# Optimization experiments

Hardware: AMD Instinct MI355X
Metric: run time of the kernel (lower is better)

Reference implementation:

```python
import jax, jax.numpy as jnp
import numpy as np

B, N, D = 1024, 32, 512  # graphs, node types (=nodes per graph), node_dim
EPS = 1e-5

def setup_inputs() -> dict:
    key = jax.random.key(0)
    ks = jax.random.split(key, 6)
    z = jax.random.normal(ks[0], (B, N, D), jnp.float32)
    # each graph contains every node type exactly once, in random order
    idx = jax.vmap(lambda k: jax.random.permutation(k, N))(jax.random.split(ks[1], B)).astype(jnp.int32)
    A = jax.random.normal(ks[2], (N, N), jnp.float32) / np.sqrt(N)
    W1 = jax.random.normal(ks[3], (N, D, 2 * D), jnp.float32) / np.sqrt(D)
    b1 = jnp.zeros((N, 2 * D), jnp.float32)
    W2 = jax.random.normal(ks[4], (N, 2 * D, D), jnp.float32) / np.sqrt(2 * D)
    b2 = jnp.zeros((N, D), jnp.float32)
    gamma = jnp.ones((D,), jnp.float32)
    beta = jnp.zeros((D,), jnp.float32)
    return dict(z=z, idx=idx, A=A, W1=W1, b1=b1, W2=W2, b2=b2, gamma=gamma, beta=beta)

def _layernorm(x, g, b):
    m = jnp.mean(x, axis=-1, keepdims=True)
    v = jnp.var(x, axis=-1, keepdims=True)
    return (x - m) * jax.lax.rsqrt(v + EPS) * g + b

def reference(z, idx, A, W1, b1, W2, b2, gamma, beta):
    # per-graph submatrix of global A: A_sub[b] = A[node_index, node_index]
    A_sub = A[idx[:, :, None], idx[:, None, :]]            # [B,K,K]
    # Az[b] = A_sub[b].T @ z[b]
    Az = jnp.einsum('bkj,bkd->bjd', A_sub, z)              # [B,K,D]
    Az = _layernorm(Az, gamma, beta)
    # route node of type t to expert t: inv[b,t] = position of type t in graph b
    inv = jnp.argsort(idx, axis=1)                         # [B,N]
    x = jnp.take_along_axis(Az, inv[:, :, None], axis=1)   # [B,N,D] type-ordered
    # per-type 2-layer MLP experts (Linear -> ELU -> Linear), dropout in eval mode
    h = jax.nn.elu(jnp.einsum('bnd,ndh->bnh', x, W1) + b1) # [B,N,2D]
    y = jnp.einsum('bnh,nhd->bnd', h, W2) + b2             # [B,N,D]
    # scatter back to node order: node j in graph b has type idx[b,j]
    mix = jnp.take_along_axis(y, idx[:, :, None].astype(jnp.int32), axis=1)
    return mix + Az
```

## Files before the change

### kernel.cpp

```cpp
#include <hip/hip_runtime.h>
#include <hip/hip_bf16.h>
#include <math.h>

#define B_  1024
#define N_  32
#define D_  512
#define EPS_ 1e-5f

typedef __attribute__((ext_vector_type(8))) short bf16x8;
typedef __attribute__((ext_vector_type(4))) float f32x4;
using bf16 = __hip_bfloat16;
typedef unsigned int u32;
typedef const u32 __attribute__((address_space(1)))* gp_t;
typedef u32 __attribute__((address_space(3)))* sp_t;

static __device__ __forceinline__ void gload16(const void* g, void* s) {
  __builtin_amdgcn_global_load_lds((gp_t)g, (sp_t)s, 16, 0, 0);
}
static __device__ __forceinline__ void bar() {
  asm volatile("s_barrier" ::: "memory");
}

static __device__ __forceinline__ unsigned short f2bf(float f) {
  union { float f; u32 u; } c; c.f = f;
  u32 r = c.u + 0x7fff + ((c.u >> 16) & 1);
  return (unsigned short)(r >> 16);
}
static __device__ __forceinline__ float bf2f(unsigned short h) {
  union { u32 u; float f; } c; c.u = ((u32)h) << 16;
  return c.f;
}

__global__ __launch_bounds__(256) void transpose_cast_kernel(
    const float* __restrict__ in, bf16* __restrict__ out, int R, int C) {
  __shared__ unsigned short tile[64][65];
  const size_t mat = (size_t)blockIdx.z * (size_t)R * (size_t)C;
  const float* inp = in + mat;
  bf16* outp = out + mat;
  const int c0 = blockIdx.x * 64, r0 = blockIdx.y * 64;
  const int tr = threadIdx.x >> 4;
  const int tc = (threadIdx.x & 15) * 4;
#pragma unroll
  for (int i = 0; i < 4; ++i) {
    const int r = tr + i * 16;
    float4 v = *(const float4*)&inp[(size_t)(r0 + r) * C + c0 + tc];
    tile[r][tc + 0] = f2bf(v.x);
    tile[r][tc + 1] = f2bf(v.y);
    tile[r][tc + 2] = f2bf(v.z);
    tile[r][tc + 3] = f2bf(v.w);
  }
  __syncthreads();
#pragma unroll
  for (int i = 0; i < 2; ++i) {
    const int chunk = i * 256 + threadIdx.x;
    const int c = chunk >> 3, r8 = (chunk & 7) * 8;
    union { bf16x8 v; unsigned short u[8]; } pk;
#pragma unroll
    for (int k = 0; k < 8; ++k) pk.u[k] = tile[r8 + k][c];
    *(bf16x8*)&outp[(size_t)(c0 + c) * R + r0 + r8] = pk.v;
  }
}

__global__ __launch_bounds__(256) void mix_ln_kernel(
    const float* __restrict__ z, const int* __restrict__ idx,
    const float* __restrict__ A, const float* __restrict__ gamma,
    const float* __restrict__ beta, bf16* __restrict__ x_ws,
    int* __restrict__ inv_ws) {
  __shared__ float As[32][32];
  __shared__ int   p[32];
  __shared__ float red1[4][32];
  __shared__ float red2[4][32];
  __shared__ float meanS[32];
  __shared__ float rstdS[32];

  const int b = blockIdx.x;
  const int t = threadIdx.x;
  const int lane = t & 63, wid = t >> 6;

  if (t < 32) {
    int v = idx[b * 32 + t];
    p[t] = v;
    inv_ws[b * 32 + v] = t;
  }
  __syncthreads();
  for (int i = t; i < 1024; i += 256) {
    int k = i >> 5, n = i & 31;
    As[k][n] = A[p[k] * 32 + n];
  }
  __syncthreads();

  const int d0 = t, d1 = t + 256;
  const float* zb = z + (size_t)b * (N_ * D_);
  float acc0[32], acc1[32];
#pragma unroll
  for (int n = 0; n < 32; ++n) { acc0[n] = 0.f; acc1[n] = 0.f; }

  for (int k = 0; k < 32; ++k) {
    float z0 = zb[k * D_ + d0];
    float z1 = zb[k * D_ + d1];
#pragma unroll
    for (int c = 0; c < 8; ++c) {
      float4 a4 = *(const float4*)&As[k][c * 4];
      acc0[c * 4 + 0] = fmaf(a4.x, z0, acc0[c * 4 + 0]);
      acc1[c * 4 + 0] = fmaf(a4.x, z1, acc1[c * 4 + 0]);
      acc0[c * 4 + 1] = fmaf(a4.y, z0, acc0[c * 4 + 1]);
      acc1[c * 4 + 1] = fmaf(a4.y, z1, acc1[c * 4 + 1]);
      acc0[c * 4 + 2] = fmaf(a4.z, z0, acc0[c * 4 + 2]);
      acc1[c * 4 + 2] = fmaf(a4.z, z1, acc1[c * 4 + 2]);
      acc0[c * 4 + 3] = fmaf(a4.w, z0, acc0[c * 4 + 3]);
      acc1[c * 4 + 3] = fmaf(a4.w, z1, acc1[c * 4 + 3]);
    }
  }

#pragma unroll
  for (int n = 0; n < 32; ++n) {
    float v1 = acc0[n] + acc1[n];
    float v2 = acc0[n] * acc0[n] + acc1[n] * acc1[n];
#pragma unroll
    for (int mk = 1; mk < 64; mk <<= 1) {
      v1 += __shfl_xor(v1, mk);
      v2 += __shfl_xor(v2, mk);
    }
    if (lane == 0) { red1[wid][n] = v1; red2[wid][n] = v2; }
  }
  __syncthreads();
  if (t < 32) {
    float S1 = red1[0][t] + red1[1][t] + red1[2][t] + red1[3][t];
    float S2 = red2[0][t] + red2[1][t] + red2[2][t] + red2[3][t];
    float mean = S1 * (1.f / D_);
    float var  = S2 * (1.f / D_) - mean * mean;
    meanS[t] = mean;
    rstdS[t] = rsqrtf(var + EPS_);
  }
  __syncthreads();

  const float g0 = gamma[d0], g1 = gamma[d1];
  const float be0 = beta[d0], be1 = beta[d1];
#pragma unroll
  for (int n = 0; n < 32; ++n) {
    float mn = meanS[n], rs = rstdS[n];
    float x0 = (acc0[n] - mn) * rs * g0 + be0;
    float x1 = (acc1[n] - mn) * rs * g1 + be1;
    size_t base = ((size_t)n * B_ + b) * D_;
    x_ws[base + d0] = __float2bfloat16(x0);
    x_ws[base + d1] = __float2bfloat16(x1);
  }
}

#define STG_A(P, H, S) do {                                                   \
    const bf16* g_ = Ag + (size_t)((H) * 128) * KD + (S) * 64 + soff;         \
    gload16(g_, Alds + (P) * 32768 + (H) * 16384 + dof);                      \
    gload16(g_ + (size_t)64 * KD, Alds + (P) * 32768 + (H) * 16384 + 8192 + dof); \
  } while (0)
#define STG_B(P, H, S) do {                                                   \
    const bf16* g_ = Bg + (size_t)((H) * 128) * KD + (S) * 64 + soff;         \
    gload16(g_, Blds + (P) * 32768 + (H) * 16384 + dof);                      \
    gload16(g_ + (size_t)64 * KD, Blds + (P) * 32768 + (H) * 16384 + 8192 + dof); \
  } while (0)

#define RD_A(P, H) do {                                                       \
    const char* Ab_ = Alds + (P) * 32768 + (H) * 16384;                       \
    _Pragma("unroll")                                                         \
    for (int fi = 0; fi < 2; ++fi) {                                          \
      av[fi][0] = *(const bf16x8*)(Ab_ + raA + fi * 2048 + j16);              \
      av[fi][1] = *(const bf16x8*)(Ab_ + raA + fi * 2048 + (j16 ^ 64));       \
    }                                                                         \
  } while (0)
#define RD_B(P, H, BV) do {                                                   \
    const char* Bb_ = Blds + (P) * 32768 + (H) * 16384;                       \
    _Pragma("unroll")                                                         \
    for (int fj = 0; fj < 4; ++fj) {                                          \
      BV[fj][0] = *(const bf16x8*)(Bb_ + raB + fj * 2048 + j16);              \
      BV[fj][1] = *(const bf16x8*)(Bb_ + raB + fj * 2048 + (j16 ^ 64));       \
    }                                                                         \
  } while (0)

#define MMA16(QR, QC, BV) do {                                                \
    __builtin_amdgcn_s_setprio(1);                                            \
    _Pragma("unroll")                                                         \
    for (int fi = 0; fi < 2; ++fi)                                            \
      _Pragma("unroll")                                                       \
      for (int fj = 0; fj < 4; ++fj) {                                        \
        acc[QR][QC][fi][fj] = __builtin_amdgcn_mfma_f32_16x16x32_bf16(        \
            av[fi][0], BV[fj][0], acc[QR][QC][fi][fj], 0, 0, 0);              \
        acc[QR][QC][fi][fj] = __builtin_amdgcn_mfma_f32_16x16x32_bf16(        \
            av[fi][1], BV[fj][1], acc[QR][QC][fi][fj], 0, 0, 0);              \
      }                                                                       \
    __builtin_amdgcn_s_setprio(0);                                            \
  } while (0)

#define VMC4() asm volatile("s_waitcnt vmcnt(4)" ::: "memory")
#define VMC0() asm volatile("s_waitcnt vmcnt(0)" ::: "memory")

template <int KD, int NS>
static __device__ __forceinline__ void gemm8_core(
    const bf16* __restrict__ Ag, const bf16* __restrict__ Bg,
    char* __restrict__ Alds, char* __restrict__ Blds,
    f32x4 (&acc)[2][2][2][4], const int t) {
  const int lane = t & 63, wid = t >> 6;
  const int llo = lane & 15, lhi = lane >> 4;
  const int raA = ((wid & 3) * 32 + llo) * 128;
  const int raB = ((wid >> 2) * 64 + llo) * 128;
  const int j16 = (lhi ^ (llo & 7)) * 16;
  const int soff = (t >> 3) * KD + ((t ^ (t >> 3)) & 7) * 8;
  const int dof = wid * 1024;

  bf16x8 av[2][2], bv0[4][2], bv1[4][2];

  STG_A(0, 0, 0); STG_B(0, 0, 0); STG_A(0, 1, 0); STG_B(0, 1, 0);
  STG_A(1, 0, 1); STG_B(1, 0, 1);
  VMC4();
  bar();

#pragma unroll 1
  for (int it = 0; it < NS / 2; ++it) {
    const int s0 = 2 * it;
    RD_A(0, 0); RD_B(0, 0, bv0);
    if (s0 + 1 < NS) STG_A(1, 1, s0 + 1);
    bar(); MMA16(0, 0, bv0); bar();
    RD_B(0, 1, bv1);
    if (s0 + 1 < NS) STG_B(1, 1, s0 + 1);
    bar(); MMA16(0, 1, bv1); bar();
    RD_A(0, 1);
    if (s0 + 2 < NS) STG_A(0, 0, s0 + 2);
    bar(); MMA16(1, 1, bv1); bar();
    if (s0 + 2 < NS) STG_B(0, 0, s0 + 2);
    bar(); MMA16(1, 0, bv0);
    if (s0 + 2 < NS) { VMC4(); } else { VMC0(); }
    bar();
    const int s1 = s0 + 1;
    RD_A(1, 0); RD_B(1, 0, bv0);
    if (s1 + 1 < NS) STG_A(0, 1, s1 + 1);
    bar(); MMA16(0, 0, bv0); bar();
    RD_B(1, 1, bv1);
    if (s1 + 1 < NS) STG_B(0, 1, s1 + 1);
    bar(); MMA16(0, 1, bv1); bar();
    RD_A(1, 1);
    if (s1 + 2 < NS) STG_A(1, 0, s1 + 2);
    bar(); MMA16(1, 1, bv1); bar();
    if (s1 + 2 < NS) STG_B(1, 0, s1 + 2);
    bar(); MMA16(1, 0, bv0);
    if (s1 + 2 < NS) { VMC4(); } else { VMC0(); }
    bar();
  }
}

__global__ __launch_bounds__(512, 2) void gemm1_kernel(
    const bf16* __restrict__ X,
    const bf16* __restrict__ W1t,
    const float* __restrict__ b1,
    bf16* __restrict__ Hout) {
  extern __shared__ char lds[];
  char* Alds = lds;
  char* Blds = lds + 65536;

  const int bid = blockIdx.x;
  const int swz = (bid & 7) * 64 + (bid >> 3);
  const int m  = swz >> 4;
  const int r_ = swz & 15;
  const int hb = r_ >> 2, bb = r_ & 3;

  const int t = threadIdx.x;
  const int lane = t & 63, wid = t >> 6;
  const int llo = lane & 15, lhi = lane >> 4;

  const bf16* Ag = W1t + (size_t)m * (1024 * 512) + (size_t)(hb * 256) * 512;
  const bf16* Bg = X   + (size_t)m * (1024 * 512) + (size_t)(bb * 256) * 512;

  const f32x4 fzero = {0.f, 0.f, 0.f, 0.f};
  f32x4 acc[2][2][2][4];
#pragma unroll
  for (int a = 0; a < 2; ++a)
#pragma unroll
    for (int b = 0; b < 2; ++b)
#pragma unroll
      for (int c = 0; c < 2; ++c)
#pragma unroll
        for (int d = 0; d < 4; ++d) acc[a][b][c][d] = fzero;

  gemm8_core<512, 8>(Ag, Bg, Alds, Blds, acc, t);

  const float* b1m = b1 + m * 1024 + hb * 256;
#pragma unroll
  for (int qr = 0; qr < 2; ++qr)
#pragma unroll
    for (int fi = 0; fi < 2; ++fi) {
      const int h_loc = qr * 128 + (wid & 3) * 32 + fi * 16 + lhi * 4;
      const float4 bi = *(const float4*)&b1m[h_loc];
#pragma unroll
      for (int qc = 0; qc < 2; ++qc)
#pragma unroll
        for (int fj = 0; fj < 4; ++fj) {
          const int b_loc = qc * 128 + (wid >> 2) * 64 + fj * 16 + llo;
          float v0 = acc[qr][qc][fi][fj][0] + bi.x;
          float v1 = acc[qr][qc][fi][fj][1] + bi.y;
          float v2 = acc[qr][qc][fi][fj][2] + bi.z;
          float v3 = acc[qr][qc][fi][fj][3] + bi.w;
          v0 = v0 > 0.f ? v0 : __expf(v0) - 1.0f;
          v1 = v1 > 0.f ? v1 : __expf(v1) - 1.0f;
          v2 = v2 > 0.f ? v2 : __expf(v2) - 1.0f;
          v3 = v3 > 0.f ? v3 : __expf(v3) - 1.0f;
          ushort4 pk;
          pk.x = f2bf(v0); pk.y = f2bf(v1); pk.z = f2bf(v2); pk.w = f2bf(v3);
          const int byte = (b_loc * 512 + h_loc * 2) ^ ((b_loc & 7) << 4);
          *(ushort4*)(lds + byte) = pk;
        }
    }
  __syncthreads();
  bf16* Hm = Hout + (size_t)m * (1024 * 1024);
  const int b0 = bb * 256, h0 = hb * 256;
#pragma unroll
  for (int r = 0; r < 16; ++r) {
    const int chunk = r * 512 + t;
    const int bl = chunk >> 5, hc = chunk & 31;
    const int byte = (bl * 512 + hc * 16) ^ ((bl & 7) << 4);
    bf16x8 v = *(const bf16x8*)(lds + byte);
    *(bf16x8*)&Hm[(size_t)(b0 + bl) * 1024 + h0 + hc * 8] = v;
  }
}

__global__ __launch_bounds__(512, 2) void gemm2_kernel(
    const bf16* __restrict__ Hin,
    const bf16* __restrict__ W2t,
    const float* __restrict__ b2,
    const bf16* __restrict__ Xb,
    const int* __restrict__ inv,
    float* __restrict__ out) {
  extern __shared__ char lds[];
  char* Alds = lds;
  char* Blds = lds + 65536;

  const int bid = blockIdx.x;
  const int swz = (bid & 7) * 32 + (bid >> 3);
  const int m  = swz >> 3;
  const int r_ = swz & 7;
  const int db_ = r_ >> 2, bb = r_ & 3;

  const int t = threadIdx.x;
  const int lane = t & 63, wid = t >> 6;
  const int llo = lane & 15, lhi = lane >> 4;

  const bf16* Ag = W2t + (size_t)m * (512 * 1024) + (size_t)(db_ * 256) * 1024;
  const bf16* Bg = Hin + (size_t)m * (1024 * 1024) + (size_t)(bb * 256) * 1024;

  const f32x4 fzero = {0.f, 0.f, 0.f, 0.f};
  f32x4 acc[2][2][2][4];
#pragma unroll
  for (int a = 0; a < 2; ++a)
#pragma unroll
    for (int b = 0; b < 2; ++b)
#pragma unroll
      for (int c = 0; c < 2; ++c)
#pragma unroll
        for (int d = 0; d < 4; ++d) acc[a][b][c][d] = fzero;

  gemm8_core<1024, 16>(Ag, Bg, Alds, Blds, acc, t);

  const float* b2m = b2 + m * 512;
  const bf16* Xm = Xb + (size_t)m * (1024 * 512);
#pragma unroll
  for (int qc = 0; qc < 2; ++qc)
#pragma unroll
    for (int fj = 0; fj < 4; ++fj) {
      const int b_ = bb * 256 + qc * 128 + (wid >> 2) * 64 + fj * 16 + llo;
      const int n_out = inv[b_ * 32 + m];
      float* orow = out + ((size_t)b_ * 32 + n_out) * 512;
      const bf16* xrow = Xm + (size_t)b_ * 512;
#pragma unroll
      for (int qr = 0; qr < 2; ++qr)
#pragma unroll
        for (int fi = 0; fi < 2; ++fi) {
          const int d0 = db_ * 256 + qr * 128 + (wid & 3) * 32 + fi * 16 + lhi * 4;
          const float4 bi = *(const float4*)&b2m[d0];
          const ushort4 xr = *(const ushort4*)&xrow[d0];
          float4 v;
          v.x = acc[qr][qc][fi][fj][0] + bi.x + bf2f(xr.x);
          v.y = acc[qr][qc][fi][fj][1] + bi.y + bf2f(xr.y);
          v.z = acc[qr][qc][fi][fj][2] + bi.z + bf2f(xr.z);
          v.w = acc[qr][qc][fi][fj][3] + bi.w + bf2f(xr.w);
          *(float4*)&orow[d0] = v;
        }
    }
}

extern "C" void kernel_launch(void* const* d_in, const int* in_sizes, int n_in,
                              void* d_out, int out_size, void* d_ws, size_t ws_size,
                              hipStream_t stream) {
  const float* z     = (const float*)d_in[0];
  const int*   idx   = (const int*)d_in[1];
  const float* A     = (const float*)d_in[2];
  const float* W1    = (const float*)d_in[3];
  const float* b1    = (const float*)d_in[4];
  const float* W2    = (const float*)d_in[5];
  const float* b2    = (const float*)d_in[6];
  const float* gamma = (const float*)d_in[7];
  const float* beta  = (const float*)d_in[8];
  float* out = (float*)d_out;
  char* ws = (char*)d_ws;

  const size_t OFF_X   = 0;
  const size_t OFF_H   = 33554432;
  const size_t OFF_W1T = 100663296;
  const size_t OFF_W2T = 134217728;
  const size_t OFF_INV = 167772160;
  const size_t NEED    = 167903232;
  if (ws_size < NEED) return;

  bf16* Xb  = (bf16*)(ws + OFF_X);
  bf16* Hb  = (bf16*)(ws + OFF_H);
  bf16* W1t = (bf16*)(ws + OFF_W1T);
  bf16* W2t = (bf16*)(ws + OFF_W2T);
  int*  inv = (int*)(ws + OFF_INV);

  hipFuncSetAttribute((const void*)gemm1_kernel,
                      hipFuncAttributeMaxDynamicSharedMemorySize, 131072);
  hipFuncSetAttribute((const void*)gemm2_kernel,
                      hipFuncAttributeMaxDynamicSharedMemorySize, 131072);

  transpose_cast_kernel<<<dim3(16, 8, 32), 256, 0, stream>>>(W1, W1t, 512, 1024);
  transpose_cast_kernel<<<dim3(8, 16, 32), 256, 0, stream>>>(W2, W2t, 1024, 512);

  mix_ln_kernel<<<dim3(B_), 256, 0, stream>>>(z, idx, A, gamma, beta, Xb, inv);

  gemm1_kernel<<<dim3(512), 512, 131072, stream>>>(Xb, W1t, b1, Hb);
  gemm2_kernel<<<dim3(256), 512, 131072, stream>>>(Hb, W2t, b2, Xb, inv, out);
}
```

Measured before the change: 182.2 us.

## Simplify GEMM pipeline to per-stage double buffering and vectorize LayerNorm kernel loads

New measurement: 189.5 us. +4.0%, slower.

```diff
diff --git a/kernel.cpp b/kernel.cpp
--- a/kernel.cpp
+++ b/kernel.cpp
@@ -89,26 +89,34 @@
   }
   __syncthreads();
 
-  const int d0 = t, d1 = t + 256;
+  const int d0 = 2 * t;
   const float* zb = z + (size_t)b * (N_ * D_);
   float acc0[32], acc1[32];
 #pragma unroll
   for (int n = 0; n < 32; ++n) { acc0[n] = 0.f; acc1[n] = 0.f; }
 
-  for (int k = 0; k < 32; ++k) {
-    float z0 = zb[k * D_ + d0];
-    float z1 = zb[k * D_ + d1];
-#pragma unroll
-    for (int c = 0; c < 8; ++c) {
-      float4 a4 = *(const float4*)&As[k][c * 4];
-      acc0[c * 4 + 0] = fmaf(a4.x, z0, acc0[c * 4 + 0]);
-      acc1[c * 4 + 0] = fmaf(a4.x, z1, acc1[c * 4 + 0]);
-      acc0[c * 4 + 1] = fmaf(a4.y, z0, acc0[c * 4 + 1]);
-      acc1[c * 4 + 1] = fmaf(a4.y, z1, acc1[c * 4 + 1]);
-      acc0[c * 4 + 2] = fmaf(a4.z, z0, acc0[c * 4 + 2]);
-      acc1[c * 4 + 2] = fmaf(a4.z, z1, acc1[c * 4 + 2]);
-      acc0[c * 4 + 3] = fmaf(a4.w, z0, acc0[c * 4 + 3]);
-      acc1[c * 4 + 3] = fmaf(a4.w, z1, acc1[c * 4 + 3]);
+  float2 zr[16];
+#pragma unroll 1
+  for (int half = 0; half < 2; ++half) {
+#pragma unroll
+    for (int kk = 0; kk < 16; ++kk)
+      zr[kk] = *(const float2*)&zb[(half * 16 + kk) * D_ + d0];
+#pragma unroll
+    for (int kk = 0; kk < 16; ++kk) {
+      const int k = half * 16 + kk;
+      const float z0 = zr[kk].x, z1 = zr[kk].y;
+#pragma unroll
+      for (int c = 0; c < 8; ++c) {
+        float4 a4 = *(const float4*)&As[k][c * 4];
+        acc0[c * 4 + 0] = fmaf(a4.x, z0, acc0[c * 4 + 0]);
+        acc1[c * 4 + 0] = fmaf(a4.x, z1, acc1[c * 4 + 0]);
+        acc0[c * 4 + 1] = fmaf(a4.y, z0, acc0[c * 4 + 1]);
+        acc1[c * 4 + 1] = fmaf(a4.y, z1, acc1[c * 4 + 1]);
+        acc0[c * 4 + 2] = fmaf(a4.z, z0, acc0[c * 4 + 2]);
+        acc1[c * 4 + 2] = fmaf(a4.z, z1, acc1[c * 4 + 2]);
+        acc0[c * 4 + 3] = fmaf(a4.w, z0, acc0[c * 4 + 3]);
+        acc1[c * 4 + 3] = fmaf(a4.w, z1, acc1[c * 4 + 3]);
+      }
     }
   }
 
@@ -134,16 +142,16 @@
   }
   __syncthreads();
 
-  const float g0 = gamma[d0], g1 = gamma[d1];
-  const float be0 = beta[d0], be1 = beta[d1];
+  const float2 g2 = *(const float2*)&gamma[d0];
+  const float2 be2 = *(const float2*)&beta[d0];
 #pragma unroll
   for (int n = 0; n < 32; ++n) {
     float mn = meanS[n], rs = rstdS[n];
-    float x0 = (acc0[n] - mn) * rs * g0 + be0;
-    float x1 = (acc1[n] - mn) * rs * g1 + be1;
+    float x0 = (acc0[n] - mn) * rs * g2.x + be2.x;
+    float x1 = (acc1[n] - mn) * rs * g2.y + be2.y;
     size_t base = ((size_t)n * B_ + b) * D_;
-    x_ws[base + d0] = __float2bfloat16(x0);
-    x_ws[base + d1] = __float2bfloat16(x1);
+    ushort2 pk; pk.x = f2bf(x0); pk.y = f2bf(x1);
+    *(ushort2*)&x_ws[base + d0] = pk;
   }
 }
 
@@ -157,13 +165,14 @@
     gload16(g_, Blds + (P) * 32768 + (H) * 16384 + dof);                      \
     gload16(g_ + (size_t)64 * KD, Blds + (P) * 32768 + (H) * 16384 + 8192 + dof); \
   } while (0)
-
-#define RD_A(P, H) do {                                                       \
+#define STG_SUB(P, S) do { STG_A(P,0,S); STG_B(P,0,S); STG_A(P,1,S); STG_B(P,1,S); } while (0)
+
+#define RD_A(P, H, AV) do {                                                   \
     const char* Ab_ = Alds + (P) * 32768 + (H) * 16384;                       \
     _Pragma("unroll")                                                         \
     for (int fi = 0; fi < 2; ++fi) {                                          \
-      av[fi][0] = *(const bf16x8*)(Ab_ + raA + fi * 2048 + j16);              \
-      av[fi][1] = *(const bf16x8*)(Ab_ + raA + fi * 2048 + (j16 ^ 64));       \
+      AV[fi][0] = *(const bf16x8*)(Ab_ + raA + fi * 2048 + j16);              \
+      AV[fi][1] = *(const bf16x8*)(Ab_ + raA + fi * 2048 + (j16 ^ 64));       \
     }                                                                         \
   } while (0)
 #define RD_B(P, H, BV) do {                                                   \
@@ -175,21 +184,19 @@
     }                                                                         \
   } while (0)
 
-#define MMA16(QR, QC, BV) do {                                                \
-    __builtin_amdgcn_s_setprio(1);                                            \
+#define MMA16(QR, QC, AV, BV) do {                                            \
     _Pragma("unroll")                                                         \
     for (int fi = 0; fi < 2; ++fi)                                            \
       _Pragma("unroll")                                                       \
       for (int fj = 0; fj < 4; ++fj) {                                        \
         acc[QR][QC][fi][fj] = __builtin_amdgcn_mfma_f32_16x16x32_bf16(        \
-            av[fi][0], BV[fj][0], acc[QR][QC][fi][fj], 0, 0, 0);              \
+            AV[fi][0], BV[fj][0], acc[QR][QC][fi][fj], 0, 0, 0);              \
         acc[QR][QC][fi][fj] = __builtin_amdgcn_mfma_f32_16x16x32_bf16(        \
-            av[fi][1], BV[fj][1], acc[QR][QC][fi][fj], 0, 0, 0);              \
+            AV[fi][1], BV[fj][1], acc[QR][QC][fi][fj], 0, 0, 0);              \
       }                                                                       \
-    __builtin_amdgcn_s_setprio(0);                                            \
   } while (0)
 
-#define VMC4() asm volatile("s_waitcnt vmcnt(4)" ::: "memory")
+#define VMC8() asm volatile("s_waitcnt vmcnt(8)" ::: "memory")
 #define VMC0() asm volatile("s_waitcnt vmcnt(0)" ::: "memory")
 
 template <int KD, int NS>
@@ -205,42 +212,26 @@
   const int soff = (t >> 3) * KD + ((t ^ (t >> 3)) & 7) * 8;
   const int dof = wid * 1024;
 
-  bf16x8 av[2][2], bv0[4][2], bv1[4][2];
-
-  STG_A(0, 0, 0); STG_B(0, 0, 0); STG_A(0, 1, 0); STG_B(0, 1, 0);
-  STG_A(1, 0, 1); STG_B(1, 0, 1);
-  VMC4();
+  bf16x8 av0[2][2], av1[2][2], bv0[4][2], bv1[4][2];
+
+  STG_SUB(0, 0);
+  STG_SUB(1, 1);
+  VMC8();
   bar();
 
-#pragma unroll 1
-  for (int it = 0; it < NS / 2; ++it) {
-    const int s0 = 2 * it;
-    RD_A(0, 0); RD_B(0, 0, bv0);
-    if (s0 + 1 < NS) STG_A(1, 1, s0 + 1);
-    bar(); MMA16(0, 0, bv0); bar();
-    RD_B(0, 1, bv1);
-    if (s0 + 1 < NS) STG_B(1, 1, s0 + 1);
-    bar(); MMA16(0, 1, bv1); bar();
-    RD_A(0, 1);
-    if (s0 + 2 < NS) STG_A(0, 0, s0 + 2);
-    bar(); MMA16(1, 1, bv1); bar();
-    if (s0 + 2 < NS) STG_B(0, 0, s0 + 2);
-    bar(); MMA16(1, 0, bv0);
-    if (s0 + 2 < NS) { VMC4(); } else { VMC0(); }
+#pragma unroll 2
+  for (int s = 0; s < NS; ++s) {
+    const int p = s & 1;
+    RD_A(p, 0, av0); RD_B(p, 0, bv0);
+    RD_A(p, 1, av1); RD_B(p, 1, bv1);
+    __builtin_amdgcn_s_setprio(1);
+    MMA16(0, 0, av0, bv0);
+    MMA16(0, 1, av0, bv1);
+    MMA16(1, 0, av1, bv0);
+    MMA16(1, 1, av1, bv1);
+    __builtin_amdgcn_s_setprio(0);
     bar();
-    const int s1 = s0 + 1;
-    RD_A(1, 0); RD_B(1, 0, bv0);
-    if (s1 + 1 < NS) STG_A(0, 1, s1 + 1);
-    bar(); MMA16(0, 0, bv0); bar();
-    RD_B(1, 1, bv1);
-    if (s1 + 1 < NS) STG_B(0, 1, s1 + 1);
-    bar(); MMA16(0, 1, bv1); bar();
-    RD_A(1, 1);
-    if (s1 + 2 < NS) STG_A(1, 0, s1 + 2);
-    bar(); MMA16(1, 1, bv1); bar();
-    if (s1 + 2 < NS) STG_B(1, 0, s1 + 2);
-    bar(); MMA16(1, 0, bv0);
-    if (s1 + 2 < NS) { VMC4(); } else { VMC0(); }
+    if (s + 2 < NS) { STG_SUB(p, s + 2); VMC8(); } else { VMC0(); }
     bar();
   }
 }
```
